# Performance work log

Measured on AMD Instinct MI355X. Metric: run time of the kernel, lower is better.

The kernel has to match this reference:

```python
import jax, jax.numpy as jnp
import numpy as np

N, E = 50000, 600000
IN, H, C = 128, 128, 10


def _glorot(key, shape):
    lim = float(np.sqrt(6.0 / (shape[0] + shape[1])))
    return jax.random.uniform(key, shape, jnp.float32, -lim, lim)


def setup_inputs() -> dict:
    key = jax.random.key(0)
    ks = jax.random.split(key, 16)
    inp = {
        "x": jax.random.normal(ks[0], (N, IN), jnp.float32),
        "edge_index": jax.random.randint(ks[1], (2, E), 0, N, jnp.int64)
        if jax.config.jax_enable_x64 else jax.random.randint(ks[1], (2, E), 0, N, jnp.int32),
        "W1": _glorot(ks[2], (IN, H)), "b1": jnp.zeros((H,), jnp.float32),
        "W2": _glorot(ks[3], (H, H)),  "b2": jnp.zeros((H,), jnp.float32),
        "W3": _glorot(ks[4], (H, H)),  "b3": jnp.zeros((H,), jnp.float32),
        "W4": _glorot(ks[5], (H, H)),  "b4": jnp.zeros((H,), jnp.float32),
        "Wm1": _glorot(ks[6], (H, H)), "bm1": jnp.zeros((H,), jnp.float32),
        "Wm2": _glorot(ks[7], (H, C)), "bm2": jnp.zeros((C,), jnp.float32),
    }
    return inp


def gcn_layer(x, W, b, src, dst):
    # PyG GCNConv: linear transform, add self-loops, symmetric normalization,
    # scatter-add aggregation to destination nodes, then bias.
    n = x.shape[0]
    xw = x @ W  # [N, H]
    # in-degree (computed on dst), +1 for self-loop
    deg = jax.ops.segment_sum(jnp.ones(src.shape[0], xw.dtype), dst, num_segments=n) + 1.0
    dinv = jax.lax.rsqrt(deg)  # deg >= 1, safe
    norm = dinv[src] * dinv[dst]  # [E]
    agg = jax.ops.segment_sum(xw[src] * norm[:, None], dst, num_segments=n)
    agg = agg + xw * (dinv * dinv)[:, None]  # self-loop messages
    return agg + b


def reference(x, edge_index, W1, b1, W2, b2, W3, b3, W4, b4, Wm1, bm1, Wm2, bm2):
    src, dst = edge_index[0], edge_index[1]
    h = jax.nn.elu(gcn_layer(x, W1, b1, src, dst))
    h = jax.nn.elu(gcn_layer(h, W2, b2, src, dst))
    h = jax.nn.elu(gcn_layer(h, W3, b3, src, dst))
    h = jax.nn.elu(gcn_layer(h, W4, b4, src, dst))
    # Faithful to the source bug: S is reassigned from the fixed `s = h` each
    # iteration, so only the last MLP layer's output survives.
    s = h
    for Wm, bm in ((Wm1, bm1), (Wm2, bm2)):
        S = jax.nn.elu(s @ Wm + bm)
    return (h, S)
```

## Files before the change

kernel.cpp:

```cpp
#include <hip/hip_runtime.h>
#include <hip/hip_bf16.h>
#include <hip/hip_fp16.h>
#include <math.h>

typedef __hip_bfloat16 bf16;
typedef __attribute__((ext_vector_type(8))) short short8;
typedef __attribute__((ext_vector_type(4))) float f32x4;

__device__ __forceinline__ float elu_f(float x){ return x > 0.f ? x : expm1f(x); }
__device__ __forceinline__ float b2f(unsigned short u){ return __uint_as_float(((unsigned)u) << 16); }
__device__ __forceinline__ unsigned short f2b(float f){ bf16 h = __float2bfloat16(f); return *reinterpret_cast<unsigned short*>(&h); }
__device__ __forceinline__ float2 h2f2(unsigned u){
    __half2 h = *reinterpret_cast<__half2*>(&u);
    return make_float2(__low2float(h), __high2float(h));
}

__device__ __forceinline__ int f_is64(const int* raw){ return raw[0] == 0; }
__device__ __forceinline__ int f_isbf(const int* raw){ return raw[1]*2 > 4096; }

__device__ __forceinline__ int load_src(const int* ei, int e, int E, int is64){
    return is64 ? ei[2*e] : ei[e];
}
__device__ __forceinline__ int load_dst(const int* ei, int e, int E, int is64){
    return is64 ? ei[2*(E + e)] : ei[E + e];
}
__device__ __forceinline__ float loadf(const void* base, size_t idx, int isbf){
    return isbf ? __bfloat162float(((const bf16*)base)[idx]) : ((const float*)base)[idx];
}

__global__ __launch_bounds__(256) void detect_part_kernel(const unsigned* __restrict__ ei_u, int twoE_words,
                                                          const unsigned* __restrict__ x_u, int min_xwords,
                                                          int* __restrict__ raw,
                                                          int* __restrict__ counts, int N){
    __shared__ int sd[256];
    __shared__ int sc[256];
    int tid = threadIdx.x;
    int gid = blockIdx.x*256 + tid;
    long long pairs = twoE_words/2;

    for (int i2 = gid; i2 < N; i2 += 32768) counts[i2] = 0;

    int orv = 0;
    if (gid < 16384 && pairs > 0){
        long long idx = ((long long)gid * pairs) / 16384;
        long long w = 2*idx + 1;
        if (w < twoE_words) orv = (int)ei_u[w];
    }
    int cnt = 0;
    int s = gid - 16384;
    if (s >= 0 && s < 4096){
        long long idx = ((long long)s * min_xwords) / 4096;
        if (idx < min_xwords){
            unsigned e = (x_u[idx] >> 7) & 0xFFu;
            cnt = (e >= 96u && e <= 160u) ? 1 : 0;
        }
    }
    sd[tid] = orv; sc[tid] = cnt;
    __syncthreads();
    #pragma unroll
    for (int off = 128; off > 0; off >>= 1){
        if (tid < off){ sd[tid] |= sd[tid+off]; sc[tid] += sc[tid+off]; }
        __syncthreads();
    }
    if (tid == 0){
        if (sd[0]) atomicOr(&raw[0], sd[0]);
        if (sc[0]) atomicAdd(&raw[1], sc[0]);
    }
}

__global__ __launch_bounds__(256) void wprep_kernel(const void* __restrict__ W0, const void* __restrict__ W1,
                                                    const void* __restrict__ W2, const void* __restrict__ W3,
                                                    const int* __restrict__ raw,
                                                    unsigned short* __restrict__ WThi, unsigned short* __restrict__ WTlo){
    int l = blockIdx.x >> 6;
    const void* Wl = l == 0 ? W0 : l == 1 ? W1 : l == 2 ? W2 : W3;
    int isbf = f_isbf(raw);
    int o = (blockIdx.x & 63)*256 + threadIdx.x;
    int c = o >> 7, k = o & 127;
    unsigned short hi, lo;
    if (isbf){
        hi = ((const unsigned short*)Wl)[k*128 + c]; lo = 0;
    } else {
        float w = ((const float*)Wl)[k*128 + c];
        hi = f2b(w);
        lo = f2b(w - b2f(hi));
    }
    WThi[(size_t)l*16384 + o] = hi;
    WTlo[(size_t)l*16384 + o] = lo;
}

__global__ void count_kernel(const int* __restrict__ ei, const int* __restrict__ raw,
                             int* __restrict__ counts, int E, int N){
    int e = blockIdx.x*256 + threadIdx.x;
    if (e < E){
        int d = load_dst(ei, e, E, f_is64(raw));
        if ((unsigned)d < (unsigned)N) atomicAdd(&counts[d], 1);
    }
}

__global__ void partial_kernel(const int* __restrict__ counts, int* __restrict__ partial, int N){
    __shared__ int sd[256];
    int tid = threadIdx.x;
    int i = blockIdx.x*256 + tid;
    sd[tid] = (i < N) ? counts[i] : 0;
    __syncthreads();
    #pragma unroll
    for (int off = 128; off > 0; off >>= 1){
        if (tid < off) sd[tid] += sd[tid+off];
        __syncthreads();
    }
    if (tid == 0) partial[blockIdx.x] = sd[0];
}

__global__ void offsets_kernel(const int* __restrict__ counts, const int* __restrict__ partial,
                               int* __restrict__ offsets, int* __restrict__ cursor,
                               float* __restrict__ dinv, int N){
    __shared__ int sd[256];
    __shared__ int sbase;
    int tid = threadIdx.x;

    int acc = 0;
    for (int i = tid; i < (int)blockIdx.x; i += 256) acc += partial[i];
    sd[tid] = acc;
    __syncthreads();
    #pragma unroll
    for (int off = 128; off > 0; off >>= 1){
        if (tid < off) sd[tid] += sd[tid+off];
        __syncthreads();
    }
    if (tid == 0) sbase = sd[0];
    __syncthreads();

    int i = blockIdx.x*256 + tid;
    int v = (i < N) ? counts[i] : 0;
    sd[tid] = v;
    __syncthreads();
    #pragma unroll
    for (int off = 1; off < 256; off <<= 1){
        int t = (tid >= off) ? sd[tid-off] : 0;
        __syncthreads();
        sd[tid] += t;
        __syncthreads();
    }
    if (i < N){
        int o = sbase + sd[tid] - v;
        offsets[i] = o;
        cursor[i]  = o;
        double d = (double)(v + 1);
        if (d < 1.0) d = 1.0;
        dinv[i] = (float)(1.0 / sqrt(d));
    }
}

__global__ void scatter_kernel(const int* __restrict__ ei, const int* __restrict__ raw,
                               int* __restrict__ cursor, int* __restrict__ csr, int E, int N){
    int e = blockIdx.x*256 + threadIdx.x;
    if (e < E){
        int is64 = f_is64(raw);
        int d = load_dst(ei, e, E, is64);
        int s = load_src(ei, e, E, is64);
        if ((unsigned)d < (unsigned)N){
            int pos = atomicAdd(&cursor[d], 1);
            if ((unsigned)pos < (unsigned)E) csr[pos] = s;
        }
    }
}

__global__ __launch_bounds__(256) void gemm_kernel(const void* __restrict__ X,
                                                   const unsigned short* __restrict__ WThi,
                                                   const unsigned short* __restrict__ WTlo,
                                                   const int* __restrict__ raw,
                                                   __half* __restrict__ Y, int N){
    __shared__ __align__(16) unsigned short xhi[64*136];
    __shared__ __align__(16) unsigned short xlo[64*136];
    __shared__ __align__(16) unsigned short bh[128*40];
    __shared__ __align__(16) unsigned short bl[128*40];
    int tid = threadIdx.x;
    int r0 = blockIdx.x*64;
    int isbf = f_isbf(raw);

    if (isbf){
        for (int i = tid; i < 64*16; i += 256){
            int r = i >> 4, sg = i & 15;
            float4 v = make_float4(0.f,0.f,0.f,0.f);
            if (r0 + r < N) v = ((const float4*)X)[(size_t)(r0+r)*16 + sg];
            *(float4*)&xhi[r*136 + sg*8] = v;
        }
    } else {
        for (int i = tid; i < 64*32; i += 256){
            int r = i >> 5, f4 = i & 31;
            float4 v = make_float4(0.f,0.f,0.f,0.f);
            if (r0 + r < N) v = ((const float4*)X)[(size_t)(r0+r)*32 + f4];
            ushort4 hv, lv;
            hv.x = f2b(v.x); lv.x = f2b(v.x - b2f(hv.x));
            hv.y = f2b(v.y); lv.y = f2b(v.y - b2f(hv.y));
            hv.z = f2b(v.z); lv.z = f2b(v.z - b2f(hv.z));
            hv.w = f2b(v.w); lv.w = f2b(v.w - b2f(hv.w));
            *(ushort4*)&xhi[r*136 + f4*4] = hv;
            *(ushort4*)&xlo[r*136 + f4*4] = lv;
        }
    }

    int wv = tid >> 6, lane = tid & 63;
    int lq = lane & 15, lh = lane >> 4;

    f32x4 acc[8];
    #pragma unroll
    for (int i = 0; i < 8; i++){
        #pragma unroll
        for (int e = 0; e < 4; e++) acc[i][e] = 0.f;
    }

    for (int k0 = 0; k0 < 4; k0++){
        __syncthreads();
        for (int i = tid; i < 512; i += 256){
            int rr = i >> 2, sg = i & 3;
            *(float4*)&bh[rr*40 + sg*8] = *(const float4*)&WThi[rr*128 + k0*32 + sg*8];
        }
        if (!isbf){
            for (int i = tid; i < 512; i += 256){
                int rr = i >> 2, sg = i & 3;
                *(float4*)&bl[rr*40 + sg*8] = *(const float4*)&WTlo[rr*128 + k0*32 + sg*8];
            }
        }
        __syncthreads();

        short8 ah = *reinterpret_cast<const short8*>(&xhi[(wv*16 + lq)*136 + k0*32 + lh*8]);
        if (isbf){
            #pragma unroll
            for (int nt = 0; nt < 8; nt++){
                short8 bhf = *reinterpret_cast<const short8*>(&bh[(nt*16 + lq)*40 + lh*8]);
                acc[nt] = __builtin_amdgcn_mfma_f32_16x16x32_bf16(ah, bhf, acc[nt], 0, 0, 0);
            }
        } else {
            short8 al = *reinterpret_cast<const short8*>(&xlo[(wv*16 + lq)*136 + k0*32 + lh*8]);
            #pragma unroll
            for (int nt = 0; nt < 8; nt++){
                short8 bhf = *reinterpret_cast<const short8*>(&bh[(nt*16 + lq)*40 + lh*8]);
                short8 blf = *reinterpret_cast<const short8*>(&bl[(nt*16 + lq)*40 + lh*8]);
                acc[nt] = __builtin_amdgcn_mfma_f32_16x16x32_bf16(ah, bhf, acc[nt], 0, 0, 0);
                acc[nt] = __builtin_amdgcn_mfma_f32_16x16x32_bf16(al, bhf, acc[nt], 0, 0, 0);
                acc[nt] = __builtin_amdgcn_mfma_f32_16x16x32_bf16(ah, blf, acc[nt], 0, 0, 0);
            }
        }
    }

    #pragma unroll
    for (int nt = 0; nt < 8; nt++){
        #pragma unroll
        for (int i = 0; i < 4; i++){
            int row = r0 + wv*16 + lh*4 + i;
            if (row < N) Y[(size_t)row*128 + nt*16 + lq] = __float2half(acc[nt][i]);
        }
    }
}

__global__ __launch_bounds__(256) void agg_kernel(const unsigned* __restrict__ XWh, const float* __restrict__ dinv,
                                                  const int* __restrict__ offsets, const int* __restrict__ counts,
                                                  const int* __restrict__ csr, const void* __restrict__ bias,
                                                  void* __restrict__ Hout, const int* __restrict__ raw, int N){
    int wave = threadIdx.x >> 6;
    int lane = threadIdx.x & 63;
    int n = blockIdx.x*4 + wave;
    if (n >= N) return;
    int isbf = f_isbf(raw);

    float dn = dinv[n];
    float sw = dn*dn;

    float2 sf = h2f2(XWh[(size_t)n*64 + lane]);
    float accx = sf.x*sw, accy = sf.y*sw;

    int j0 = offsets[n], cnt = counts[n];
    for (int base = 0; base < cnt; base += 64){
        int m = cnt - base; if (m > 64) m = 64;
        int s_l = 0; float w_l = 0.f;
        if (lane < m){
            int s = csr[j0 + base + lane];
            if ((unsigned)s < (unsigned)N){ s_l = s; w_l = dinv[s]*dn; }
        }
        int j = 0;
        for (; j + 4 <= m; j += 4){
            int   s0 = __shfl(s_l, j),   s1 = __shfl(s_l, j+1), s2 = __shfl(s_l, j+2), s3 = __shfl(s_l, j+3);
            float w0 = __shfl(w_l, j),   w1 = __shfl(w_l, j+1), w2 = __shfl(w_l, j+2), w3 = __shfl(w_l, j+3);
            unsigned u0 = XWh[(size_t)s0*64 + lane];
            unsigned u1 = XWh[(size_t)s1*64 + lane];
            unsigned u2 = XWh[(size_t)s2*64 + lane];
            unsigned u3 = XWh[(size_t)s3*64 + lane];
            float2 f0 = h2f2(u0), f1 = h2f2(u1), f2 = h2f2(u2), f3 = h2f2(u3);
            accx += f0.x*w0; accy += f0.y*w0;
            accx += f1.x*w1; accy += f1.y*w1;
            accx += f2.x*w2; accy += f2.y*w2;
            accx += f3.x*w3; accy += f3.y*w3;
        }
        for (; j < m; ++j){
            int   s = __shfl(s_l, j);
            float w = __shfl(w_l, j);
            float2 f = h2f2(XWh[(size_t)s*64 + lane]);
            accx += f.x*w; accy += f.y*w;
        }
    }

    accx = elu_f(accx + loadf(bias, 2*lane,     isbf));
    accy = elu_f(accy + loadf(bias, 2*lane + 1, isbf));
    if (isbf){
        ushort2 o;
        o.x = f2b(accx); o.y = f2b(accy);
        *(ushort2*)((bf16*)Hout + (size_t)n*128 + lane*2) = o;
    } else {
        *(float2*)((float*)Hout + (size_t)n*128 + lane*2) = make_float2(accx, accy);
    }
}

__global__ __launch_bounds__(256) void mlp_kernel(void* __restrict__ dout, const void* __restrict__ Wm,
                                                  const void* __restrict__ bm, const int* __restrict__ raw, int N){
    __shared__ float ws_[1280];
    __shared__ __align__(16) float hs[16][136];
    int tid = threadIdx.x;
    int isbf = f_isbf(raw);
    for (int i = tid; i < 1280; i += 256) ws_[i] = loadf(Wm, i, isbf);

    int r = tid >> 4, c = tid & 15;
    int row = blockIdx.x*16 + r;
    if (isbf){
        if (row < N){
            float4 v = ((const float4*)dout)[(size_t)row*16 + c];
            const unsigned short* u = (const unsigned short*)&v;
            #pragma unroll
            for (int j = 0; j < 8; j++) hs[r][c*8 + j] = b2f(u[j]);
        }
    } else {
        if (row < N){
            float4 v0 = ((const float4*)dout)[(size_t)row*32 + c*2];
            float4 v1 = ((const float4*)dout)[(size_t)row*32 + c*2 + 1];
            *(float4*)&hs[r][c*8]     = v0;
            *(float4*)&hs[r][c*8 + 4] = v1;
        }
    }
    __syncthreads();
    if (row < N && c < 10){
        float acc = 0.f;
        #pragma unroll 8
        for (int k = 0; k < 128; k++) acc += hs[r][k]*ws_[k*10 + c];
        acc += loadf(bm, c, isbf);
        float res = elu_f(acc);
        if (isbf){
            ((bf16*)dout)[(size_t)N*128 + (size_t)row*10 + c] = __float2bfloat16(res);
        } else {
            ((float*)dout)[(size_t)N*128 + (size_t)row*10 + c] = res;
        }
    }
}

static inline char* alignup(char* p, size_t a){ return (char*)(((uintptr_t)p + a - 1) & ~(a - 1)); }

extern "C" void kernel_launch(void* const* d_in, const int* in_sizes, int n_in,
                              void* d_out, int out_size, void* d_ws, size_t ws_size,
                              hipStream_t stream){
    const void* x  = d_in[0];
    const int*  ei = (const int*)d_in[1];
    const void* W[4] = {d_in[2], d_in[4], d_in[6], d_in[8]};
    const void* B[4] = {d_in[3], d_in[5], d_in[7], d_in[9]};
    const void* Wm2 = d_in[12];
    const void* bm2 = d_in[13];

    int N = in_sizes[0] / 128;
    int E = in_sizes[1] / 2;

    char* p = (char*)d_ws;
    int*   raw      = (int*)p;                     p = alignup(p + 4*sizeof(int), 256);
    float* dinv     = (float*)p;                   p = alignup(p + (size_t)N*4, 256);
    int*   counts   = (int*)p;                     p = alignup(p + (size_t)N*4, 256);
    int*   offsets  = (int*)p;                     p = alignup(p + (size_t)N*4, 256);
    int*   cursor   = (int*)p;                     p = alignup(p + (size_t)N*4, 256);
    int*   partial  = (int*)p;                     p = alignup(p + 256*4, 256);
    int*   csr      = (int*)p;                     p = alignup(p + (size_t)E*4, 256);
    __half* xw      = (__half*)p;                  p = alignup(p + (size_t)N*128*4, 256);
    unsigned short* WThi = (unsigned short*)p;     p = alignup(p + (size_t)4*16384*2, 256);
    unsigned short* WTlo = (unsigned short*)p;     p = alignup(p + (size_t)4*16384*2, 256);

    int nb = (N + 255)/256;

    hipMemsetAsync(raw, 0, 4*sizeof(int), stream);
    detect_part_kernel<<<128, 256, 0, stream>>>((const unsigned*)ei, 2*E, (const unsigned*)x, N*128/2, raw, counts, N);
    wprep_kernel  <<<256, 256, 0, stream>>>(W[0], W[1], W[2], W[3], raw, WThi, WTlo);
    count_kernel  <<<(E + 255)/256, 256, 0, stream>>>(ei, raw, counts, E, N);
    partial_kernel<<<nb, 256, 0, stream>>>(counts, partial, N);
    offsets_kernel<<<nb, 256, 0, stream>>>(counts, partial, offsets, cursor, dinv, N);
    scatter_kernel<<<(E + 255)/256, 256, 0, stream>>>(ei, raw, cursor, csr, E, N);

    for (int l = 0; l < 4; ++l){
        const void* Xin = (l == 0) ? x : (const void*)d_out;
        gemm_kernel<<<(N + 63)/64, 256, 0, stream>>>(Xin, WThi + (size_t)l*16384, WTlo + (size_t)l*16384, raw, xw, N);
        agg_kernel <<<(N + 3)/4, 256, 0, stream>>>((const unsigned*)xw, dinv, offsets, counts, csr, B[l], d_out, raw, N);
    }
    mlp_kernel<<<((N*16) + 255)/256, 256, 0, stream>>>(d_out, Wm2, bm2, raw, N);
}
```

Measured before the change: 408.3 us.

## Store intermediate activations in fp16, load GEMM A-fragments directly, double-buffer weights

Hidden activations of layers 1-3 are now written to a separate fp16 buffer instead of the fp32 output, halving activation traffic between the aggregation and the next GEMM. The GEMM now loads A fragments straight from global memory into registers, dropping the shared-memory staging, and double-buffers the weight tiles to cut syncs. The partial-sum kernel is removed: each offsets block instead sums all earlier counts directly. The fp16 intermediates can lose precision compared with the fp32 path, though the hi/lo split is kept for fp16 inputs. The redundant prefix summation also grows quadratically with the number of blocks.

```diff
diff --git a/kernel.cpp b/kernel.cpp
--- a/kernel.cpp
+++ b/kernel.cpp
@@ -98,29 +98,17 @@
     }
 }
 
-__global__ void partial_kernel(const int* __restrict__ counts, int* __restrict__ partial, int N){
-    __shared__ int sd[256];
-    int tid = threadIdx.x;
-    int i = blockIdx.x*256 + tid;
-    sd[tid] = (i < N) ? counts[i] : 0;
-    __syncthreads();
-    #pragma unroll
-    for (int off = 128; off > 0; off >>= 1){
-        if (tid < off) sd[tid] += sd[tid+off];
-        __syncthreads();
-    }
-    if (tid == 0) partial[blockIdx.x] = sd[0];
-}
-
-__global__ void offsets_kernel(const int* __restrict__ counts, const int* __restrict__ partial,
+__global__ void offsets_kernel(const int* __restrict__ counts,
                                int* __restrict__ offsets, int* __restrict__ cursor,
                                float* __restrict__ dinv, int N){
     __shared__ int sd[256];
     __shared__ int sbase;
     int tid = threadIdx.x;
 
+    int lim = (int)blockIdx.x*256;
+    if (lim > N) lim = N;
     int acc = 0;
-    for (int i = tid; i < (int)blockIdx.x; i += 256) acc += partial[i];
+    for (int i = tid; i < lim; i += 256) acc += counts[i];
     sd[tid] = acc;
     __syncthreads();
     #pragma unroll
@@ -169,40 +157,68 @@
 __global__ __launch_bounds__(256) void gemm_kernel(const void* __restrict__ X,
                                                    const unsigned short* __restrict__ WThi,
                                                    const unsigned short* __restrict__ WTlo,
-                                                   const int* __restrict__ raw,
+                                                   const int* __restrict__ raw, int in_mode,
                                                    __half* __restrict__ Y, int N){
-    __shared__ __align__(16) unsigned short xhi[64*136];
-    __shared__ __align__(16) unsigned short xlo[64*136];
-    __shared__ __align__(16) unsigned short bh[128*40];
-    __shared__ __align__(16) unsigned short bl[128*40];
+    __shared__ __align__(16) unsigned short bh[2][128*40];
+    __shared__ __align__(16) unsigned short bl[2][128*40];
     int tid = threadIdx.x;
     int r0 = blockIdx.x*64;
     int isbf = f_isbf(raw);
-
-    if (isbf){
-        for (int i = tid; i < 64*16; i += 256){
-            int r = i >> 4, sg = i & 15;
-            float4 v = make_float4(0.f,0.f,0.f,0.f);
-            if (r0 + r < N) v = ((const float4*)X)[(size_t)(r0+r)*16 + sg];
-            *(float4*)&xhi[r*136 + sg*8] = v;
-        }
-    } else {
-        for (int i = tid; i < 64*32; i += 256){
-            int r = i >> 5, f4 = i & 31;
-            float4 v = make_float4(0.f,0.f,0.f,0.f);
-            if (r0 + r < N) v = ((const float4*)X)[(size_t)(r0+r)*32 + f4];
-            ushort4 hv, lv;
-            hv.x = f2b(v.x); lv.x = f2b(v.x - b2f(hv.x));
-            hv.y = f2b(v.y); lv.y = f2b(v.y - b2f(hv.y));
-            hv.z = f2b(v.z); lv.z = f2b(v.z - b2f(hv.z));
-            hv.w = f2b(v.w); lv.w = f2b(v.w - b2f(hv.w));
-            *(ushort4*)&xhi[r*136 + f4*4] = hv;
-            *(ushort4*)&xlo[r*136 + f4*4] = lv;
-        }
-    }
+    int single = (in_mode == 0) && isbf;
 
     int wv = tid >> 6, lane = tid & 63;
     int lq = lane & 15, lh = lane >> 4;
+    int arow = r0 + wv*16 + lq;
+    bool rowok = arow < N;
+
+    short8 ah[4], al[4];
+    #pragma unroll
+    for (int k0 = 0; k0 < 4; k0++){
+        #pragma unroll
+        for (int j = 0; j < 8; j++){ ah[k0][j] = 0; al[k0][j] = 0; }
+    }
+    if (rowok){
+        if (in_mode == 1){
+            #pragma unroll
+            for (int k0 = 0; k0 < 4; k0++){
+                float4 v = ((const float4*)X)[(size_t)arow*16 + k0*4 + lh];
+                const __half* hp = (const __half*)&v;
+                #pragma unroll
+                for (int j = 0; j < 8; j++){
+                    float f = __half2float(hp[j]);
+                    unsigned short hi = f2b(f);
+                    ah[k0][j] = (short)hi;
+                    al[k0][j] = (short)f2b(f - b2f(hi));
+                }
+            }
+        } else if (isbf){
+            #pragma unroll
+            for (int k0 = 0; k0 < 4; k0++){
+                float4 v = ((const float4*)X)[(size_t)arow*16 + k0*4 + lh];
+                ah[k0] = *reinterpret_cast<const short8*>(&v);
+            }
+        } else {
+            #pragma unroll
+            for (int k0 = 0; k0 < 4; k0++){
+                float4 v0 = ((const float4*)X)[(size_t)arow*32 + k0*8 + lh*2];
+                float4 v1 = ((const float4*)X)[(size_t)arow*32 + k0*8 + lh*2 + 1];
+                const float* fp = (const float*)&v0;
+                #pragma unroll
+                for (int j = 0; j < 4; j++){
+                    unsigned short hi = f2b(fp[j]);
+                    ah[k0][j] = (short)hi;
+                    al[k0][j] = (short)f2b(fp[j] - b2f(hi));
+                }
+                const float* fq = (const float*)&v1;
+                #pragma unroll
+                for (int j = 0; j < 4; j++){
+                    unsigned short hi = f2b(fq[j]);
+                    ah[k0][4+j] = (short)hi;
+                    al[k0][4+j] = (short)f2b(fq[j] - b2f(hi));
+                }
+            }
+        }
+    }
 
     f32x4 acc[8];
     #pragma unroll
@@ -211,38 +227,52 @@
         for (int e = 0; e < 4; e++) acc[i][e] = 0.f;
     }
 
-    for (int k0 = 0; k0 < 4; k0++){
-        __syncthreads();
+    {
         for (int i = tid; i < 512; i += 256){
             int rr = i >> 2, sg = i & 3;
-            *(float4*)&bh[rr*40 + sg*8] = *(const float4*)&WThi[rr*128 + k0*32 + sg*8];
-        }
-        if (!isbf){
+            *(float4*)&bh[0][rr*40 + sg*8] = *(const float4*)&WThi[rr*128 + 0*32 + sg*8];
+        }
+        if (!single){
             for (int i = tid; i < 512; i += 256){
                 int rr = i >> 2, sg = i & 3;
-                *(float4*)&bl[rr*40 + sg*8] = *(const float4*)&WTlo[rr*128 + k0*32 + sg*8];
+                *(float4*)&bl[0][rr*40 + sg*8] = *(const float4*)&WTlo[rr*128 + 0*32 + sg*8];
+            }
+        }
+    }
+    __syncthreads();
+
+    for (int k0 = 0; k0 < 4; k0++){
+        int buf = k0 & 1;
+        if (k0 < 3){
+            int nbuf = buf ^ 1, kn = k0 + 1;
+            for (int i = tid; i < 512; i += 256){
+                int rr = i >> 2, sg = i & 3;
+                *(float4*)&bh[nbuf][rr*40 + sg*8] = *(const float4*)&WThi[rr*128 + kn*32 + sg*8];
+            }
+            if (!single){
+                for (int i = tid; i < 512; i += 256){
+                    int rr = i >> 2, sg = i & 3;
+                    *(float4*)&bl[nbuf][rr*40 + sg*8] = *(const float4*)&WTlo[rr*128 + kn*32 + sg*8];
+                }
+            }
+        }
+        if (single){
+            #pragma unroll
+            for (int nt = 0; nt < 8; nt++){
+                short8 bhf = *reinterpret_cast<const short8*>(&bh[buf][(nt*16 + lq)*40 + lh*8]);
+                acc[nt] = __builtin_amdgcn_mfma_f32_16x16x32_bf16(ah[k0], bhf, acc[nt], 0, 0, 0);
+            }
+        } else {
+            #pragma unroll
+            for (int nt = 0; nt < 8; nt++){
+                short8 bhf = *reinterpret_cast<const short8*>(&bh[buf][(nt*16 + lq)*40 + lh*8]);
+                short8 blf = *reinterpret_cast<const short8*>(&bl[buf][(nt*16 + lq)*40 + lh*8]);
+                acc[nt] = __builtin_amdgcn_mfma_f32_16x16x32_bf16(ah[k0], bhf, acc[nt], 0, 0, 0);
+                acc[nt] = __builtin_amdgcn_mfma_f32_16x16x32_bf16(al[k0], bhf, acc[nt], 0, 0, 0);
+                acc[nt] = __builtin_amdgcn_mfma_f32_16x16x32_bf16(ah[k0], blf, acc[nt], 0, 0, 0);
             }
         }
         __syncthreads();
-
-        short8 ah = *reinterpret_cast<const short8*>(&xhi[(wv*16 + lq)*136 + k0*32 + lh*8]);
-        if (isbf){
-            #pragma unroll
-            for (int nt = 0; nt < 8; nt++){
-                short8 bhf = *reinterpret_cast<const short8*>(&bh[(nt*16 + lq)*40 + lh*8]);
-                acc[nt] = __builtin_amdgcn_mfma_f32_16x16x32_bf16(ah, bhf, acc[nt], 0, 0, 0);
-            }
-        } else {
-            short8 al = *reinterpret_cast<const short8*>(&xlo[(wv*16 + lq)*136 + k0*32 + lh*8]);
-            #pragma unroll
-            for (int nt = 0; nt < 8; nt++){
-                short8 bhf = *reinterpret_cast<const short8*>(&bh[(nt*16 + lq)*40 + lh*8]);
-                short8 blf = *reinterpret_cast<const short8*>(&bl[(nt*16 + lq)*40 + lh*8]);
-                acc[nt] = __builtin_amdgcn_mfma_f32_16x16x32_bf16(ah, bhf, acc[nt], 0, 0, 0);
-                acc[nt] = __builtin_amdgcn_mfma_f32_16x16x32_bf16(al, bhf, acc[nt], 0, 0, 0);
-                acc[nt] = __builtin_amdgcn_mfma_f32_16x16x32_bf16(ah, blf, acc[nt], 0, 0, 0);
-            }
-        }
     }
 
     #pragma unroll
@@ -258,7 +288,8 @@
 __global__ __launch_bounds__(256) void agg_kernel(const unsigned* __restrict__ XWh, const float* __restrict__ dinv,
                                                   const int* __restrict__ offsets, const int* __restrict__ counts,
                                                   const int* __restrict__ csr, const void* __restrict__ bias,
-                                                  void* __restrict__ Hout, const int* __restrict__ raw, int N){
+                                                  void* __restrict__ Hout, const int* __restrict__ raw,
+                                                  int out16, int N){
     int wave = threadIdx.x >> 6;
     int lane = threadIdx.x & 63;
     int n = blockIdx.x*4 + wave;
@@ -303,7 +334,12 @@
 
     accx = elu_f(accx + loadf(bias, 2*lane,     isbf));
     accy = elu_f(accy + loadf(bias, 2*lane + 1, isbf));
-    if (isbf){
+    if (out16){
+        __half2 o;
+        o.x = __float2half(accx);
+        o.y = __float2half(accy);
+        *(__half2*)((__half*)Hout + (size_t)n*128 + lane*2) = o;
+    } else if (isbf){
         ushort2 o;
         o.x = f2b(accx); o.y = f2b(accy);
         *(ushort2*)((bf16*)Hout + (size_t)n*128 + lane*2) = o;
@@ -373,9 +409,9 @@
     int*   counts   = (int*)p;                     p = alignup(p + (size_t)N*4, 256);
     int*   offsets  = (int*)p;                     p = alignup(p + (size_t)N*4, 256);
     int*   cursor   = (int*)p;                     p = alignup(p + (size_t)N*4, 256);
-    int*   partial  = (int*)p;                     p = alignup(p + 256*4, 256);
     int*   csr      = (int*)p;                     p = alignup(p + (size_t)E*4, 256);
-    __half* xw      = (__half*)p;                  p = alignup(p + (size_t)N*128*4, 256);
+    __half* xw      = (__half*)p;                  p = alignup(p + (size_t)N*128*2, 256);
+    __half* hbuf    = (__half*)p;                  p = alignup(p + (size_t)N*128*2, 256);
     unsigned short* WThi = (unsigned short*)p;     p = alignup(p + (size_t)4*16384*2, 256);
     unsigned short* WTlo = (unsigned short*)p;     p = alignup(p + (size_t)4*16384*2, 256);
 
@@ -385,14 +421,16 @@
     detect_part_kernel<<<128, 256, 0, stream>>>((const unsigned*)ei, 2*E, (const unsigned*)x, N*128/2, raw, counts, N);
     wprep_kernel  <<<256, 256, 0, stream>>>(W[0], W[1], W[2], W[3], raw, WThi, WTlo);
     count_kernel  <<<(E + 255)/256, 256, 0, stream>>>(ei, raw, counts, E, N);
-    partial_kernel<<<nb, 256, 0, stream>>>(counts, partial, N);
-    offsets_kernel<<<nb, 256, 0, stream>>>(counts, partial, offsets, cursor, dinv, N);
+    offsets_kernel<<<nb, 256, 0, stream>>>(counts, offsets, cursor, dinv, N);
     scatter_kernel<<<(E + 255)/256, 256, 0, stream>>>(ei, raw, cursor, csr, E, N);
 
     for (int l = 0; l < 4; ++l){
-        const void* Xin = (l == 0) ? x : (const void*)d_out;
-        gemm_kernel<<<(N + 63)/64, 256, 0, stream>>>(Xin, WThi + (size_t)l*16384, WTlo + (size_t)l*16384, raw, xw, N);
-        agg_kernel <<<(N + 3)/4, 256, 0, stream>>>((const unsigned*)xw, dinv, offsets, counts, csr, B[l], d_out, raw, N);
+        const void* Xin = (l == 0) ? x : (const void*)hbuf;
+        int in_mode = (l == 0) ? 0 : 1;
+        int out16   = (l < 3) ? 1 : 0;
+        void* Hout  = (l < 3) ? (void*)hbuf : d_out;
+        gemm_kernel<<<(N + 63)/64, 256, 0, stream>>>(Xin, WThi + (size_t)l*16384, WTlo + (size_t)l*16384, raw, in_mode, xw, N);
+        agg_kernel <<<(N + 3)/4, 256, 0, stream>>>((const unsigned*)xw, dinv, offsets, counts, csr, B[l], Hout, raw, out16, N);
     }
     mlp_kernel<<<((N*16) + 255)/256, 256, 0, stream>>>(d_out, Wm2, bm2, raw, N);
 }
```

New measurement: 412.3 us. No clear change (+1.0%).

## Fuse MLP head into last aggregation, store fp16 intermediates, drop partial-scan kernel

Applied to the files above, without the earlier changes.

Three changes. The final Wm2 MLP is computed inside the last aggregation kernel using wave shuffles, which removes a separate kernel and a re-read of the hidden features. Hidden activations from layers 1-3 are stored as fp16 in a scratch buffer instead of d_out, halving their write and read traffic, and the next GEMM splits each fp16 value into bf16 hi/lo parts. The partial-sum kernel is removed: each offsets block now re-sums all preceding counts directly, which adds redundant reads (quadratic in block count) in exchange for one fewer launch. Storing intermediates in fp16 lowers precision, and on fp32 inputs the GEMMs already ran the three-MFMA split path.

```diff
diff --git a/kernel.cpp b/kernel.cpp
--- a/kernel.cpp
+++ b/kernel.cpp
@@ -98,29 +98,17 @@
     }
 }
 
-__global__ void partial_kernel(const int* __restrict__ counts, int* __restrict__ partial, int N){
-    __shared__ int sd[256];
-    int tid = threadIdx.x;
-    int i = blockIdx.x*256 + tid;
-    sd[tid] = (i < N) ? counts[i] : 0;
-    __syncthreads();
-    #pragma unroll
-    for (int off = 128; off > 0; off >>= 1){
-        if (tid < off) sd[tid] += sd[tid+off];
-        __syncthreads();
-    }
-    if (tid == 0) partial[blockIdx.x] = sd[0];
-}
-
-__global__ void offsets_kernel(const int* __restrict__ counts, const int* __restrict__ partial,
+__global__ void offsets_kernel(const int* __restrict__ counts,
                                int* __restrict__ offsets, int* __restrict__ cursor,
                                float* __restrict__ dinv, int N){
     __shared__ int sd[256];
     __shared__ int sbase;
     int tid = threadIdx.x;
 
+    int lim = (int)blockIdx.x*256;
+    if (lim > N) lim = N;
     int acc = 0;
-    for (int i = tid; i < (int)blockIdx.x; i += 256) acc += partial[i];
+    for (int i = tid; i < lim; i += 256) acc += counts[i];
     sd[tid] = acc;
     __syncthreads();
     #pragma unroll
@@ -169,7 +157,7 @@
 __global__ __launch_bounds__(256) void gemm_kernel(const void* __restrict__ X,
                                                    const unsigned short* __restrict__ WThi,
                                                    const unsigned short* __restrict__ WTlo,
-                                                   const int* __restrict__ raw,
+                                                   const int* __restrict__ raw, int in_mode,
                                                    __half* __restrict__ Y, int N){
     __shared__ __align__(16) unsigned short xhi[64*136];
     __shared__ __align__(16) unsigned short xlo[64*136];
@@ -178,13 +166,30 @@
     int tid = threadIdx.x;
     int r0 = blockIdx.x*64;
     int isbf = f_isbf(raw);
-
-    if (isbf){
+    int single = (in_mode == 0) && isbf;
+
+    if (single){
         for (int i = tid; i < 64*16; i += 256){
             int r = i >> 4, sg = i & 15;
             float4 v = make_float4(0.f,0.f,0.f,0.f);
             if (r0 + r < N) v = ((const float4*)X)[(size_t)(r0+r)*16 + sg];
             *(float4*)&xhi[r*136 + sg*8] = v;
+        }
+    } else if (in_mode == 1){
+        for (int i = tid; i < 64*16; i += 256){
+            int r = i >> 4, sg = i & 15;
+            float4 v = make_float4(0.f,0.f,0.f,0.f);
+            if (r0 + r < N) v = ((const float4*)X)[(size_t)(r0+r)*16 + sg];
+            const __half* hp = (const __half*)&v;
+            unsigned short hh[8], ll[8];
+            #pragma unroll
+            for (int j = 0; j < 8; j++){
+                float f = __half2float(hp[j]);
+                hh[j] = f2b(f);
+                ll[j] = f2b(f - b2f(hh[j]));
+            }
+            *(float4*)&xhi[r*136 + sg*8] = *(const float4*)hh;
+            *(float4*)&xlo[r*136 + sg*8] = *(const float4*)ll;
         }
     } else {
         for (int i = tid; i < 64*32; i += 256){
@@ -217,7 +222,7 @@
             int rr = i >> 2, sg = i & 3;
             *(float4*)&bh[rr*40 + sg*8] = *(const float4*)&WThi[rr*128 + k0*32 + sg*8];
         }
-        if (!isbf){
+        if (!single){
             for (int i = tid; i < 512; i += 256){
                 int rr = i >> 2, sg = i & 3;
                 *(float4*)&bl[rr*40 + sg*8] = *(const float4*)&WTlo[rr*128 + k0*32 + sg*8];
@@ -226,7 +231,7 @@
         __syncthreads();
 
         short8 ah = *reinterpret_cast<const short8*>(&xhi[(wv*16 + lq)*136 + k0*32 + lh*8]);
-        if (isbf){
+        if (single){
             #pragma unroll
             for (int nt = 0; nt < 8; nt++){
                 short8 bhf = *reinterpret_cast<const short8*>(&bh[(nt*16 + lq)*40 + lh*8]);
@@ -258,12 +263,24 @@
 __global__ __launch_bounds__(256) void agg_kernel(const unsigned* __restrict__ XWh, const float* __restrict__ dinv,
                                                   const int* __restrict__ offsets, const int* __restrict__ counts,
                                                   const int* __restrict__ csr, const void* __restrict__ bias,
-                                                  void* __restrict__ Hout, const int* __restrict__ raw, int N){
-    int wave = threadIdx.x >> 6;
-    int lane = threadIdx.x & 63;
+                                                  void* __restrict__ Hout, const int* __restrict__ raw,
+                                                  int out16, int fuse_mlp,
+                                                  const void* __restrict__ Wm, const void* __restrict__ bm, int N){
+    __shared__ float ws_[1280];
+    __shared__ float bs_[10];
+    int tid = threadIdx.x;
+    int isbf = f_isbf(raw);
+
+    if (fuse_mlp){
+        for (int i = tid; i < 1280; i += 256) ws_[i] = loadf(Wm, i, isbf);
+        if (tid < 10) bs_[tid] = loadf(bm, tid, isbf);
+        __syncthreads();
+    }
+
+    int wave = tid >> 6;
+    int lane = tid & 63;
     int n = blockIdx.x*4 + wave;
     if (n >= N) return;
-    int isbf = f_isbf(raw);
 
     float dn = dinv[n];
     float sw = dn*dn;
@@ -303,51 +320,36 @@
 
     accx = elu_f(accx + loadf(bias, 2*lane,     isbf));
     accy = elu_f(accy + loadf(bias, 2*lane + 1, isbf));
-    if (isbf){
+
+    if (out16){
+        __half2 o;
+        o.x = __float2half(accx);
+        o.y = __float2half(accy);
+        *(__half2*)((__half*)Hout + (size_t)n*128 + lane*2) = o;
+    } else if (isbf){
         ushort2 o;
         o.x = f2b(accx); o.y = f2b(accy);
         *(ushort2*)((bf16*)Hout + (size_t)n*128 + lane*2) = o;
     } else {
         *(float2*)((float*)Hout + (size_t)n*128 + lane*2) = make_float2(accx, accy);
     }
-}
-
-__global__ __launch_bounds__(256) void mlp_kernel(void* __restrict__ dout, const void* __restrict__ Wm,
-                                                  const void* __restrict__ bm, const int* __restrict__ raw, int N){
-    __shared__ float ws_[1280];
-    __shared__ __align__(16) float hs[16][136];
-    int tid = threadIdx.x;
-    int isbf = f_isbf(raw);
-    for (int i = tid; i < 1280; i += 256) ws_[i] = loadf(Wm, i, isbf);
-
-    int r = tid >> 4, c = tid & 15;
-    int row = blockIdx.x*16 + r;
-    if (isbf){
-        if (row < N){
-            float4 v = ((const float4*)dout)[(size_t)row*16 + c];
-            const unsigned short* u = (const unsigned short*)&v;
+
+    if (fuse_mlp){
+        float sval = 0.f;
+        #pragma unroll
+        for (int c = 0; c < 10; c++){
+            float pc = accx*ws_[(2*lane)*10 + c] + accy*ws_[(2*lane + 1)*10 + c];
             #pragma unroll
-            for (int j = 0; j < 8; j++) hs[r][c*8 + j] = b2f(u[j]);
-        }
-    } else {
-        if (row < N){
-            float4 v0 = ((const float4*)dout)[(size_t)row*32 + c*2];
-            float4 v1 = ((const float4*)dout)[(size_t)row*32 + c*2 + 1];
-            *(float4*)&hs[r][c*8]     = v0;
-            *(float4*)&hs[r][c*8 + 4] = v1;
-        }
-    }
-    __syncthreads();
-    if (row < N && c < 10){
-        float acc = 0.f;
-        #pragma unroll 8
-        for (int k = 0; k < 128; k++) acc += hs[r][k]*ws_[k*10 + c];
-        acc += loadf(bm, c, isbf);
-        float res = elu_f(acc);
-        if (isbf){
-            ((bf16*)dout)[(size_t)N*128 + (size_t)row*10 + c] = __float2bfloat16(res);
-        } else {
-            ((float*)dout)[(size_t)N*128 + (size_t)row*10 + c] = res;
+            for (int off = 32; off > 0; off >>= 1) pc += __shfl_xor(pc, off);
+            if (lane == c) sval = pc;
+        }
+        if (lane < 10){
+            float r = elu_f(sval + bs_[lane]);
+            if (isbf){
+                ((bf16*)Hout)[(size_t)N*128 + (size_t)n*10 + lane] = __float2bfloat16(r);
+            } else {
+                ((float*)Hout)[(size_t)N*128 + (size_t)n*10 + lane] = r;
+            }
         }
     }
 }
@@ -373,9 +375,9 @@
     int*   counts   = (int*)p;                     p = alignup(p + (size_t)N*4, 256);
     int*   offsets  = (int*)p;                     p = alignup(p + (size_t)N*4, 256);
     int*   cursor   = (int*)p;                     p = alignup(p + (size_t)N*4, 256);
-    int*   partial  = (int*)p;                     p = alignup(p + 256*4, 256);
     int*   csr      = (int*)p;                     p = alignup(p + (size_t)E*4, 256);
-    __half* xw      = (__half*)p;                  p = alignup(p + (size_t)N*128*4, 256);
+    __half* xw      = (__half*)p;                  p = alignup(p + (size_t)N*128*2, 256);
+    __half* hbuf    = (__half*)p;                  p = alignup(p + (size_t)N*128*2, 256);
     unsigned short* WThi = (unsigned short*)p;     p = alignup(p + (size_t)4*16384*2, 256);
     unsigned short* WTlo = (unsigned short*)p;     p = alignup(p + (size_t)4*16384*2, 256);
 
@@ -385,14 +387,17 @@
     detect_part_kernel<<<128, 256, 0, stream>>>((const unsigned*)ei, 2*E, (const unsigned*)x, N*128/2, raw, counts, N);
     wprep_kernel  <<<256, 256, 0, stream>>>(W[0], W[1], W[2], W[3], raw, WThi, WTlo);
     count_kernel  <<<(E + 255)/256, 256, 0, stream>>>(ei, raw, counts, E, N);
-    partial_kernel<<<nb, 256, 0, stream>>>(counts, partial, N);
-    offsets_kernel<<<nb, 256, 0, stream>>>(counts, partial, offsets, cursor, dinv, N);
+    offsets_kernel<<<nb, 256, 0, stream>>>(counts, offsets, cursor, dinv, N);
     scatter_kernel<<<(E + 255)/256, 256, 0, stream>>>(ei, raw, cursor, csr, E, N);
 
     for (int l = 0; l < 4; ++l){
-        const void* Xin = (l == 0) ? x : (const void*)d_out;
-        gemm_kernel<<<(N + 63)/64, 256, 0, stream>>>(Xin, WThi + (size_t)l*16384, WTlo + (size_t)l*16384, raw, xw, N);
-        agg_kernel <<<(N + 3)/4, 256, 0, stream>>>((const unsigned*)xw, dinv, offsets, counts, csr, B[l], d_out, raw, N);
-    }
-    mlp_kernel<<<((N*16) + 255)/256, 256, 0, stream>>>(d_out, Wm2, bm2, raw, N);
-}
+        const void* Xin = (l == 0) ? x : (const void*)hbuf;
+        int in_mode = (l == 0) ? 0 : 1;
+        int out16   = (l < 3) ? 1 : 0;
+        int fusem   = (l == 3) ? 1 : 0;
+        void* Hout  = (l < 3) ? (void*)hbuf : d_out;
+        gemm_kernel<<<(N + 63)/64, 256, 0, stream>>>(Xin, WThi + (size_t)l*16384, WTlo + (size_t)l*16384, raw, in_mode, xw, N);
+        agg_kernel <<<(N + 3)/4, 256, 0, stream>>>((const unsigned*)xw, dinv, offsets, counts, csr, B[l], Hout, raw,
+                                                   out16, fusem, Wm2, bm2, N);
+    }
+}
```

Result: slower. 444.1 us (+8.8%).
